# Kernel optimization log

Hardware: AMD Instinct MI355X
Metric: run time of the kernel (lower is better)

## Reference

```python
import jax, jax.numpy as jnp
import numpy as np

B = 4096
IND = 512
OUTD = 512
DEG = 2
P = 2  # dim_treat
KNOTS = [[0.33, 0.66], [0.33, 0.66]]
D = DEG + 1 + len(KNOTS[0])  # 5 basis functions per treatment dim


def setup_inputs() -> dict:
    key = jax.random.key(0)
    k1, k2, k3 = jax.random.split(key, 3)
    x = jax.random.uniform(k1, (B, P + IND), dtype=jnp.float32)  # treat dims in [0,1]
    weight = jax.random.uniform(k2, (IND, OUTD, D ** P), dtype=jnp.float32)  # torch.rand init
    bias = jax.random.uniform(k3, (OUTD, D ** P), dtype=jnp.float32)
    return {"x": x, "weight": weight, "bias": bias}


def _truncated_power_basis(x_treat):
    # x_treat: [B, P] -> basis: [B, P, D]
    knots = jnp.asarray(KNOTS, dtype=x_treat.dtype)  # [P, n_knots]
    # polynomial part: 1, x, x^2, ... x^DEG
    pows = jnp.stack([x_treat ** i for i in range(DEG + 1)], axis=-1)  # [B, P, DEG+1]
    # truncated part: relu(x - knot)^DEG  (DEG > 1 branch of original code)
    trunc = jax.nn.relu(x_treat[:, :, None] - knots[None, :, :]) ** DEG  # [B, P, n_knots]
    return jnp.concatenate([pows, trunc], axis=-1)


def reference(x, weight, bias):
    x_treat = x[:, :P]          # [B, P]
    x_feature = x[:, P:]        # [B, IND]
    basis = _truncated_power_basis(x_treat)  # [B, P, D]
    # Kronecker product across the two treatment dims: outer product, flattened
    kb = jnp.einsum('bi,bj->bij', basis[:, 0, :], basis[:, 1, :]).reshape(x.shape[0], D * P * 0 + D * D)  # [B, D^2]
    # fused: (weight^T @ x_feature) contracted with the per-sample basis coefficients
    out = jnp.einsum('bi,iod,bd->bo', x_feature, weight, kb)  # [B, OUTD]
    out = out + kb @ bias.T      # bias also varies with treatment basis
    out = jax.nn.relu(out)       # act='relu'
    # islastlayer=0: re-attach treatment dims
    return jnp.concatenate([x_treat, out], axis=1)  # [B, P + OUTD]
```

## Files before the change

kernel.cpp:

```cpp
#include <hip/hip_runtime.h>
#include <hip/hip_bf16.h>
#include <string.h>

#define NB    4096
#define IND_  512
#define OUTD_ 512
#define XCOLS 514
#define ND    25
#define KTOT  12800
#define KT2B  12928
#define NSPL  4

#define BM 128
#define BN 128
#define BKB 128

#define PWI 64
#define PWO 4
#define PWC (PWO * ND)
#define T8P 112

typedef float  f32x4  __attribute__((ext_vector_type(4)));
typedef int    i32x4  __attribute__((ext_vector_type(4)));
typedef int    i32x8  __attribute__((ext_vector_type(8)));
typedef unsigned short u16x4 __attribute__((ext_vector_type(4)));
typedef unsigned int   u32x2 __attribute__((ext_vector_type(2)));

__device__ __forceinline__ unsigned short f2bf(float f) {
  unsigned int x = __float_as_uint(f);
  return (unsigned short)((x + 0x7fffu + ((x >> 16) & 1u)) >> 16);
}

__device__ __forceinline__ float bf2f(unsigned short u) {
  return __uint_as_float(((unsigned int)u) << 16);
}

__device__ __forceinline__ unsigned int pk_bf16(float a, float b) {
  return (unsigned int)f2bf(a) | ((unsigned int)f2bf(b) << 16);
}

__device__ __forceinline__ unsigned char f2fp8(float v) {
  if (v < 0.015625f) {
    return (unsigned char)__float2int_rn(v * 512.0f);
  }
  unsigned int u = __float_as_uint(v);
  u += 0x7ffffu + ((u >> 20) & 1u);
  int e = (int)(u >> 23) - 127 + 7;
  unsigned int m = (u >> 20) & 7u;
  return (unsigned char)((e << 3) | m);
}

__device__ __forceinline__ float basis_f(float t, int j) {
  switch (j) {
    case 0: return 1.0f;
    case 1: return t;
    case 2: return t * t;
    case 3: { float r = t - 0.33f; r = r > 0.0f ? r : 0.0f; return r * r; }
    default:{ float r = t - 0.66f; r = r > 0.0f ? r : 0.0f; return r * r; }
  }
}

__device__ __forceinline__ void gload_lds16(const void* g, void* l) {
  __builtin_amdgcn_global_load_lds(
      (const __attribute__((address_space(1))) void*)g,
      (__attribute__((address_space(3))) void*)l, 16, 0, 0);
}

__device__ __forceinline__ void drain_all() {
  asm volatile("s_waitcnt vmcnt(0) lgkmcnt(0)" ::: "memory");
}

__global__ __launch_bounds__(256) void prep_all_kernel(
    const float* __restrict__ x, const float* __restrict__ W,
    const float* __restrict__ bias, unsigned char* __restrict__ Xf8,
    float* __restrict__ kb, unsigned char* __restrict__ kbT8,
    unsigned char* __restrict__ Wf8, float* __restrict__ out)
{
  __shared__ unsigned char tile8[PWI * T8P];
  const int bid = blockIdx.x;
  const int tid = threadIdx.x;

  if (bid < 512) {
    const int lane = tid & 63;
    #pragma unroll
    for (int rr = 0; rr < 2; ++rr) {
      const int b = bid * 8 + (tid >> 6) * 2 + rr;
      const float* xr = x + (size_t)b * XCOLS;
      const float* fp = xr + 2 + lane * 8;
      float2 a0 = *(const float2*)(fp + 0);
      float2 a1 = *(const float2*)(fp + 2);
      float2 a2 = *(const float2*)(fp + 4);
      float2 a3 = *(const float2*)(fp + 6);
      float xf[8] = {a0.x, a0.y, a1.x, a1.y, a2.x, a2.y, a3.x, a3.y};
      u32x2 pk;
      pk[0] = (unsigned int)f2fp8(xf[0]) | ((unsigned int)f2fp8(xf[1]) << 8) |
              ((unsigned int)f2fp8(xf[2]) << 16) | ((unsigned int)f2fp8(xf[3]) << 24);
      pk[1] = (unsigned int)f2fp8(xf[4]) | ((unsigned int)f2fp8(xf[5]) << 8) |
              ((unsigned int)f2fp8(xf[6]) << 16) | ((unsigned int)f2fp8(xf[7]) << 24);
      *reinterpret_cast<u32x2*>(Xf8 + (size_t)b * IND_ + lane * 8) = pk;

      float t0 = xr[0], t1 = xr[1];
      if (lane < 2) out[(size_t)b * XCOLS + lane] = (lane == 0) ? t0 : t1;
      {
        int d1 = lane / 5, d2 = lane - d1 * 5;
        float kv = basis_f(t0, d1) * basis_f(t1, d2);
        if (lane < ND) kb[(size_t)b * ND + lane] = kv;
      }
      {
        int ta = 2 * lane, tb = 2 * lane + 1;
        unsigned char ba = 0, bb = 0;
        if (ta < ND) { int d1 = ta / 5, d2 = ta - d1 * 5;
                       ba = f2fp8(basis_f(t0, d1) * basis_f(t1, d2)); }
        if (tb < ND) { int d1 = tb / 5, d2 = tb - d1 * 5;
                       bb = f2fp8(basis_f(t0, d1) * basis_f(t1, d2)); }
        *(unsigned short*)(kbT8 + (size_t)b * 128 + 2 * lane) =
            (unsigned short)ba | ((unsigned short)bb << 8);
      }
    }
  } else {
    const int pw = bid - 512;
    const int i0 = (pw & 7) * PWI;
    const int o0 = (pw >> 3) * PWO;

    for (int t = tid; t < PWI * (PWC / 4); t += 256) {
      int il = t / (PWC / 4);
      int c4 = t - il * (PWC / 4);
      float4 v = *(const float4*)(W + ((size_t)(i0 + il) * OUTD_ + o0) * ND + c4 * 4);
      unsigned int pk = (unsigned int)f2fp8(v.x) | ((unsigned int)f2fp8(v.y) << 8) |
                        ((unsigned int)f2fp8(v.z) << 16) | ((unsigned int)f2fp8(v.w) << 24);
      *(unsigned int*)&tile8[il * T8P + c4 * 4] = pk;
    }
    __syncthreads();

    for (int g = tid; g < PWC * (PWI / 8); g += 256) {
      int c  = g >> 3;
      int ig = g & 7;
      int d  = c % 25;
      int o_l = c / 25;
      unsigned long long v = 0;
      #pragma unroll
      for (int jj = 0; jj < 8; ++jj)
        v |= (unsigned long long)tile8[(ig * 8 + jj) * T8P + c] << (8 * jj);
      size_t rowb = (size_t)(o0 + o_l) * KT2B + (size_t)d * IND_ + i0;
      *reinterpret_cast<unsigned long long*>(Wf8 + rowb + ig * 8) = v;
    }

    if ((pw & 7) == 0) {
      int o = o0 + (tid >> 6);
      int p = tid & 63;
      int ta = 2 * p, tb = 2 * p + 1;
      unsigned char ba = (ta < ND) ? f2fp8(bias[o * ND + ta]) : (unsigned char)0;
      unsigned char bb = (tb < ND) ? f2fp8(bias[o * ND + tb]) : (unsigned char)0;
      *(unsigned short*)(Wf8 + (size_t)o * KT2B + KTOT + 2 * p) =
          (unsigned short)ba | ((unsigned short)bb << 8);
    }
  }
}

__global__ __launch_bounds__(256, 2) void gemm_mx_kernel(
    const unsigned char* __restrict__ Wf8, const unsigned char* __restrict__ Xf8,
    const float* __restrict__ kb, const unsigned char* __restrict__ kbT8,
    unsigned short* __restrict__ Pb)
{
  __shared__ unsigned char Als[2][BM * BKB];
  __shared__ unsigned char Bls[2][BN * BKB];

  const int tid  = threadIdx.x;
  const int lane = tid & 63;
  const int w    = tid >> 6;
  const int l15  = lane & 15;
  const int quad = lane >> 4;

  const int id  = blockIdx.x;
  const int xcd = id & 7;
  const int j   = id >> 3;
  const int bx  = j & 3;
  const int pg  = xcd * 16 + (j >> 2);
  const int by  = pg & 31;
  const int bz  = pg >> 5;

  const int o0 = bx * BM;
  const int b0 = by * BN;
  const int ks_begin = bz * 3200;
  const int ks_end   = (bz == 3) ? KT2B : ks_begin + 3200;
  const int nIter    = (ks_end - ks_begin) / BKB;

  const int o_off = (w & 1) * 64;
  const int b_off = (w >> 1) * 64;
  const int srow  = lane >> 3;
  const int scol  = ((lane & 7) ^ srow) * 16;
  const int r7    = l15 & 7;
  const int s0    = ((2 * quad) ^ r7) * 16;
  const int s1    = ((2 * quad + 1) ^ r7) * 16;

  f32x4 acc[4][4], fin[4][4];
  #pragma unroll
  for (int i = 0; i < 4; ++i)
    #pragma unroll
    for (int jj = 0; jj < 4; ++jj) { acc[i][jj] = (f32x4)0.0f; fin[i][jj] = (f32x4)0.0f; }

  float kv[4] = {1.0f, 1.0f, 1.0f, 1.0f};
  int cur_d = -1;

  auto issueAB = [&](int k0, int buf) {
    const int dd = k0 >> 9;
    #pragma unroll
    for (int c = 0; c < 4; ++c) {
      int chunk = w * 4 + c;
      int r = chunk * 8 + srow;
      gload_lds16(Wf8 + (size_t)(o0 + r) * KT2B + k0 + scol, &Als[buf][chunk * 1024]);
      const unsigned char* gb = (dd < ND)
          ? Xf8 + (size_t)(b0 + r) * IND_ + (k0 & 511) + scol
          : kbT8 + (size_t)(b0 + r) * 128 + scol;
      gload_lds16(gb, &Bls[buf][chunk * 1024]);
    }
  };

  issueAB(ks_begin, 0);
  drain_all();
  __syncthreads();

  for (int n = 0; n < nIter; ++n) {
    const int k0 = ks_begin + n * BKB;
    const int p  = n & 1;
    const int q  = p ^ 1;

    if (n + 1 < nIter) issueAB(k0 + BKB, q);

    const int d = k0 >> 9;
    if (d != cur_d) {
      if (cur_d >= 0) {
        #pragma unroll
        for (int nf = 0; nf < 4; ++nf)
          #pragma unroll
          for (int mf = 0; mf < 4; ++mf)
            #pragma unroll
            for (int r = 0; r < 4; ++r) {
              fin[mf][nf][r] += kv[nf] * acc[mf][nf][r];
              acc[mf][nf][r] = 0.0f;
            }
      }
      cur_d = d;
      if (d < ND) {
        #pragma unroll
        for (int nf = 0; nf < 4; ++nf)
          kv[nf] = kb[(size_t)(b0 + b_off + nf * 16 + l15) * ND + d];
      } else {
        #pragma unroll
        for (int nf = 0; nf < 4; ++nf) kv[nf] = 1.0f;
      }
    }

    {
      i32x8 af[4], bfr[4];
      #pragma unroll
      for (int mf = 0; mf < 4; ++mf) {
        int rb = (o_off + mf * 16 + l15) * BKB;
        i32x4 lo = *reinterpret_cast<const i32x4*>(&Als[p][rb + s0]);
        i32x4 hi = *reinterpret_cast<const i32x4*>(&Als[p][rb + s1]);
        i32x8 v;
        v[0] = lo[0]; v[1] = lo[1]; v[2] = lo[2]; v[3] = lo[3];
        v[4] = hi[0]; v[5] = hi[1]; v[6] = hi[2]; v[7] = hi[3];
        af[mf] = v;
      }
      #pragma unroll
      for (int nf = 0; nf < 4; ++nf) {
        int rb = (b_off + nf * 16 + l15) * BKB;
        i32x4 lo = *reinterpret_cast<const i32x4*>(&Bls[p][rb + s0]);
        i32x4 hi = *reinterpret_cast<const i32x4*>(&Bls[p][rb + s1]);
        i32x8 v;
        v[0] = lo[0]; v[1] = lo[1]; v[2] = lo[2]; v[3] = lo[3];
        v[4] = hi[0]; v[5] = hi[1]; v[6] = hi[2]; v[7] = hi[3];
        bfr[nf] = v;
      }
      #pragma unroll
      for (int mf = 0; mf < 4; ++mf)
        #pragma unroll
        for (int nf = 0; nf < 4; ++nf)
          acc[mf][nf] = __builtin_amdgcn_mfma_scale_f32_16x16x128_f8f6f4(
              af[mf], bfr[nf], acc[mf][nf],
              0, 0, 0, 0x7f7f7f7f, 0, 0x7f7f7f7f);
    }

    drain_all();
    __syncthreads();
  }

  #pragma unroll
  for (int nf = 0; nf < 4; ++nf)
    #pragma unroll
    for (int mf = 0; mf < 4; ++mf)
      #pragma unroll
      for (int r = 0; r < 4; ++r)
        fin[mf][nf][r] += kv[nf] * acc[mf][nf][r];

  unsigned short* Pz = Pb + (size_t)bz * NB * OUTD_;
  #pragma unroll
  for (int mf = 0; mf < 4; ++mf)
    #pragma unroll
    for (int nf = 0; nf < 4; ++nf) {
      int bg = b0 + b_off + nf * 16 + l15;
      int og = o0 + o_off + mf * 16 + quad * 4;
      u32x2 pk;
      pk[0] = pk_bf16(fin[mf][nf][0], fin[mf][nf][1]);
      pk[1] = pk_bf16(fin[mf][nf][2], fin[mf][nf][3]);
      *reinterpret_cast<u32x2*>(&Pz[(size_t)bg * OUTD_ + og]) = pk;
    }
}

__global__ __launch_bounds__(256) void epilogue_kernel(
    const unsigned short* __restrict__ Pb, float* __restrict__ out)
{
  const int idx = (blockIdx.x * 256 + threadIdx.x) * 4;
  const int b = idx >> 9;
  const int o = idx & 511;
  const size_t ps = (size_t)NB * OUTD_;
  float s[4] = {0.0f, 0.0f, 0.0f, 0.0f};
  #pragma unroll
  for (int z = 0; z < NSPL; ++z) {
    u16x4 v = *reinterpret_cast<const u16x4*>(&Pb[z * ps + idx]);
    #pragma unroll
    for (int e = 0; e < 4; ++e) s[e] += bf2f(v[e]);
  }
  float* op = out + (size_t)b * XCOLS + 2 + o;
  float2 lo, hi;
  lo.x = s[0] > 0.0f ? s[0] : 0.0f;
  lo.y = s[1] > 0.0f ? s[1] : 0.0f;
  hi.x = s[2] > 0.0f ? s[2] : 0.0f;
  hi.y = s[3] > 0.0f ? s[3] : 0.0f;
  *(float2*)op = lo;
  *(float2*)(op + 2) = hi;
}

extern "C" void kernel_launch(void* const* d_in, const int* in_sizes, int n_in,
                              void* d_out, int out_size, void* d_ws, size_t ws_size,
                              hipStream_t stream) {
  const float* x    = (const float*)d_in[0];
  const float* W    = (const float*)d_in[1];
  const float* bias = (const float*)d_in[2];
  float* out = (float*)d_out;
  char* ws = (char*)d_ws;

  const size_t xf_off  = 0;
  const size_t wf_off  = 2097152;
  const size_t kb_off  = wf_off + (size_t)OUTD_ * KT2B;
  const size_t kbt_off = kb_off + 409600;
  const size_t p_off   = kbt_off + (size_t)NB * 128;
  unsigned char* Xf8  = (unsigned char*)(ws + xf_off);
  unsigned char* Wf8  = (unsigned char*)(ws + wf_off);
  float* kb           = (float*)(ws + kb_off);
  unsigned char* kbT8 = (unsigned char*)(ws + kbt_off);
  unsigned short* Pb  = (unsigned short*)(ws + p_off);

  prep_all_kernel<<<1536, 256, 0, stream>>>(x, W, bias, Xf8, kb, kbT8, Wf8, out);
  gemm_mx_kernel<<<512, 256, 0, stream>>>(Wf8, Xf8, kb, kbT8, Pb);
  epilogue_kernel<<<(NB * OUTD_) / 1024, 256, 0, stream>>>(Pb, out);
}
```

Measured before the change: 127.3 us.

## Enlarge GEMM tile to 256x128 with 512 threads and peel bias tail

```diff
diff --git a/kernel.cpp b/kernel.cpp
--- a/kernel.cpp
+++ b/kernel.cpp
@@ -11,7 +11,7 @@
 #define KT2B  12928
 #define NSPL  4
 
-#define BM 128
+#define BM 256
 #define BN 128
 #define BKB 128
 
@@ -157,7 +157,7 @@
   }
 }
 
-__global__ __launch_bounds__(256, 2) void gemm_mx_kernel(
+__global__ __launch_bounds__(512, 2) void gemm_mx_kernel(
     const unsigned char* __restrict__ Wf8, const unsigned char* __restrict__ Xf8,
     const float* __restrict__ kb, const unsigned char* __restrict__ kbT8,
     unsigned short* __restrict__ Pb)
@@ -173,26 +173,36 @@
 
   const int id  = blockIdx.x;
   const int xcd = id & 7;
-  const int j   = id >> 3;
-  const int bx  = j & 3;
-  const int pg  = xcd * 16 + (j >> 2);
-  const int by  = pg & 31;
-  const int bz  = pg >> 5;
+  const int bx  = xcd & 1;
+  const int bz  = xcd >> 1;
+  const int by  = id >> 3;
 
   const int o0 = bx * BM;
   const int b0 = by * BN;
   const int ks_begin = bz * 3200;
-  const int ks_end   = (bz == 3) ? KT2B : ks_begin + 3200;
-  const int nIter    = (ks_end - ks_begin) / BKB;
-
-  const int o_off = (w & 1) * 64;
-  const int b_off = (w >> 1) * 64;
+  const bool tail = (bz == 3);
+
+  const int o_off = (w & 3) * 64;
+  const int b_off = (w >> 2) * 64;
   const int srow  = lane >> 3;
   const int scol  = ((lane & 7) ^ srow) * 16;
   const int r7    = l15 & 7;
   const int s0    = ((2 * quad) ^ r7) * 16;
   const int s1    = ((2 * quad + 1) ^ r7) * 16;
 
+  const unsigned char* aRow[4];
+  #pragma unroll
+  for (int c = 0; c < 4; ++c)
+    aRow[c] = Wf8 + (size_t)(o0 + (w * 4 + c) * 8 + srow) * KT2B + scol;
+  const unsigned char* bRow[2];
+  #pragma unroll
+  for (int c = 0; c < 2; ++c)
+    bRow[c] = Xf8 + (size_t)(b0 + (w * 2 + c) * 8 + srow) * IND_ + scol;
+  const unsigned char* tRow[2];
+  #pragma unroll
+  for (int c = 0; c < 2; ++c)
+    tRow[c] = kbT8 + (size_t)(b0 + (w * 2 + c) * 8 + srow) * 128 + scol;
+
   f32x4 acc[4][4], fin[4][4];
   #pragma unroll
   for (int i = 0; i < 4; ++i)
@@ -202,32 +212,39 @@
   float kv[4] = {1.0f, 1.0f, 1.0f, 1.0f};
   int cur_d = -1;
 
-  auto issueAB = [&](int k0, int buf) {
-    const int dd = k0 >> 9;
-    #pragma unroll
-    for (int c = 0; c < 4; ++c) {
-      int chunk = w * 4 + c;
-      int r = chunk * 8 + srow;
-      gload_lds16(Wf8 + (size_t)(o0 + r) * KT2B + k0 + scol, &Als[buf][chunk * 1024]);
-      const unsigned char* gb = (dd < ND)
-          ? Xf8 + (size_t)(b0 + r) * IND_ + (k0 & 511) + scol
-          : kbT8 + (size_t)(b0 + r) * 128 + scol;
-      gload_lds16(gb, &Bls[buf][chunk * 1024]);
-    }
+  auto issueAB = [&](int ao, int bcol, int buf) {
+    #pragma unroll
+    for (int c = 0; c < 4; ++c)
+      gload_lds16(aRow[c] + ao, &Als[buf][(w * 4 + c) * 1024]);
+    #pragma unroll
+    for (int c = 0; c < 2; ++c)
+      gload_lds16(bRow[c] + bcol, &Bls[buf][(w * 2 + c) * 1024]);
   };
 
-  issueAB(ks_begin, 0);
+  int ao   = ks_begin;
+  int bcol = ks_begin & 511;
+  issueAB(ao, bcol, 0);
   drain_all();
   __syncthreads();
 
-  for (int n = 0; n < nIter; ++n) {
-    const int k0 = ks_begin + n * BKB;
-    const int p  = n & 1;
-    const int q  = p ^ 1;
-
-    if (n + 1 < nIter) issueAB(k0 + BKB, q);
-
-    const int d = k0 >> 9;
+  for (int n = 0; n < 25; ++n) {
+    const int p = n & 1;
+    const int q = p ^ 1;
+
+    if (n < 24) {
+      ao += BKB;
+      bcol = (bcol + BKB) & 511;
+      issueAB(ao, bcol, q);
+    } else if (tail) {
+      #pragma unroll
+      for (int c = 0; c < 4; ++c)
+        gload_lds16(aRow[c] + KTOT, &Als[q][(w * 4 + c) * 1024]);
+      #pragma unroll
+      for (int c = 0; c < 2; ++c)
+        gload_lds16(tRow[c], &Bls[q][(w * 2 + c) * 1024]);
+    }
+
+    const int d = (ks_begin + n * BKB) >> 9;
     if (d != cur_d) {
       if (cur_d >= 0) {
         #pragma unroll
@@ -241,14 +258,9 @@
             }
       }
       cur_d = d;
-      if (d < ND) {
-        #pragma unroll
-        for (int nf = 0; nf < 4; ++nf)
-          kv[nf] = kb[(size_t)(b0 + b_off + nf * 16 + l15) * ND + d];
-      } else {
-        #pragma unroll
-        for (int nf = 0; nf < 4; ++nf) kv[nf] = 1.0f;
-      }
+      #pragma unroll
+      for (int nf = 0; nf < 4; ++nf)
+        kv[nf] = kb[(size_t)(b0 + b_off + nf * 16 + l15) * ND + d];
     }
 
     {
@@ -293,6 +305,37 @@
       #pragma unroll
       for (int r = 0; r < 4; ++r)
         fin[mf][nf][r] += kv[nf] * acc[mf][nf][r];
+
+  if (tail) {
+    i32x8 af[4], bfr[4];
+    #pragma unroll
+    for (int mf = 0; mf < 4; ++mf) {
+      int rb = (o_off + mf * 16 + l15) * BKB;
+      i32x4 lo = *reinterpret_cast<const i32x4*>(&Als[1][rb + s0]);
+      i32x4 hi = *reinterpret_cast<const i32x4*>(&Als[1][rb + s1]);
+      i32x8 v;
+      v[0] = lo[0]; v[1] = lo[1]; v[2] = lo[2]; v[3] = lo[3];
+      v[4] = hi[0]; v[5] = hi[1]; v[6] = hi[2]; v[7] = hi[3];
+      af[mf] = v;
+    }
+    #pragma unroll
+    for (int nf = 0; nf < 4; ++nf) {
+      int rb = (b_off + nf * 16 + l15) * BKB;
+      i32x4 lo = *reinterpret_cast<const i32x4*>(&Bls[1][rb + s0]);
+      i32x4 hi = *reinterpret_cast<const i32x4*>(&Bls[1][rb + s1]);
+      i32x8 v;
+      v[0] = lo[0]; v[1] = lo[1]; v[2] = lo[2]; v[3] = lo[3];
+      v[4] = hi[0]; v[5] = hi[1]; v[6] = hi[2]; v[7] = hi[3];
+      bfr[nf] = v;
+    }
+    #pragma unroll
+    for (int mf = 0; mf < 4; ++mf)
+      #pragma unroll
+      for (int nf = 0; nf < 4; ++nf)
+        fin[mf][nf] = __builtin_amdgcn_mfma_scale_f32_16x16x128_f8f6f4(
+            af[mf], bfr[nf], fin[mf][nf],
+            0, 0, 0, 0x7f7f7f7f, 0, 0x7f7f7f7f);
+  }
 
   unsigned short* Pz = Pb + (size_t)bz * NB * OUTD_;
   #pragma unroll
@@ -353,6 +396,6 @@
   unsigned short* Pb  = (unsigned short*)(ws + p_off);
 
   prep_all_kernel<<<1536, 256, 0, stream>>>(x, W, bias, Xf8, kb, kbT8, Wf8, out);
-  gemm_mx_kernel<<<512, 256, 0, stream>>>(Wf8, Xf8, kb, kbT8, Pb);
+  gemm_mx_kernel<<<256, 512, 0, stream>>>(Wf8, Xf8, kb, kbT8, Pb);
   epilogue_kernel<<<(NB * OUTD_) / 1024, 256, 0, stream>>>(Pb, out);
 }
```

New measurement: 130.3 us. 1.02x slower.

## Hold X tile in registers, split K by input chunk, use differenced basis weights

Applied to the files above, without the earlier changes.

```diff
diff --git a/kernel.cpp b/kernel.cpp
--- a/kernel.cpp
+++ b/kernel.cpp
@@ -11,9 +11,8 @@
 #define KT2B  12928
 #define NSPL  4
 
-#define BM 128
+#define BM 256
 #define BN 128
-#define BKB 128
 
 #define PWI 64
 #define PWO 4
@@ -60,20 +59,10 @@
   }
 }
 
-__device__ __forceinline__ void gload_lds16(const void* g, void* l) {
-  __builtin_amdgcn_global_load_lds(
-      (const __attribute__((address_space(1))) void*)g,
-      (__attribute__((address_space(3))) void*)l, 16, 0, 0);
-}
-
-__device__ __forceinline__ void drain_all() {
-  asm volatile("s_waitcnt vmcnt(0) lgkmcnt(0)" ::: "memory");
-}
-
 __global__ __launch_bounds__(256) void prep_all_kernel(
     const float* __restrict__ x, const float* __restrict__ W,
     const float* __restrict__ bias, unsigned char* __restrict__ Xf8,
-    float* __restrict__ kb, unsigned char* __restrict__ kbT8,
+    float* __restrict__ kbDT, unsigned char* __restrict__ kbT8,
     unsigned char* __restrict__ Wf8, float* __restrict__ out)
 {
   __shared__ unsigned char tile8[PWI * T8P];
@@ -103,8 +92,13 @@
       if (lane < 2) out[(size_t)b * XCOLS + lane] = (lane == 0) ? t0 : t1;
       {
         int d1 = lane / 5, d2 = lane - d1 * 5;
-        float kv = basis_f(t0, d1) * basis_f(t1, d2);
-        if (lane < ND) kb[(size_t)b * ND + lane] = kv;
+        float kvd = basis_f(t0, d1) * basis_f(t1, d2);
+        float kvn = 0.0f;
+        if (lane < 24) {
+          int e1 = (lane + 1) / 5, e2 = (lane + 1) - e1 * 5;
+          kvn = basis_f(t0, e1) * basis_f(t1, e2);
+        }
+        if (lane < ND) kbDT[(size_t)lane * NB + b] = kvd - kvn;
       }
       {
         int ta = 2 * lane, tb = 2 * lane + 1;
@@ -157,14 +151,11 @@
   }
 }
 
-__global__ __launch_bounds__(256, 2) void gemm_mx_kernel(
+__global__ __launch_bounds__(512, 2) void gemm_mx_kernel(
     const unsigned char* __restrict__ Wf8, const unsigned char* __restrict__ Xf8,
-    const float* __restrict__ kb, const unsigned char* __restrict__ kbT8,
+    const float* __restrict__ kbDT, const unsigned char* __restrict__ kbT8,
     unsigned short* __restrict__ Pb)
 {
-  __shared__ unsigned char Als[2][BM * BKB];
-  __shared__ unsigned char Bls[2][BN * BKB];
-
   const int tid  = threadIdx.x;
   const int lane = tid & 63;
   const int w    = tid >> 6;
@@ -172,135 +163,114 @@
   const int quad = lane >> 4;
 
   const int id  = blockIdx.x;
-  const int xcd = id & 7;
-  const int j   = id >> 3;
-  const int bx  = j & 3;
-  const int pg  = xcd * 16 + (j >> 2);
-  const int by  = pg & 31;
-  const int bz  = pg >> 5;
+  const int bx  = id & 1;
+  const int iw  = (id >> 1) & 3;
+  const int by  = id >> 3;
 
   const int o0 = bx * BM;
   const int b0 = by * BN;
-  const int ks_begin = bz * 3200;
-  const int ks_end   = (bz == 3) ? KT2B : ks_begin + 3200;
-  const int nIter    = (ks_end - ks_begin) / BKB;
-
-  const int o_off = (w & 1) * 64;
-  const int b_off = (w >> 1) * 64;
-  const int srow  = lane >> 3;
-  const int scol  = ((lane & 7) ^ srow) * 16;
-  const int r7    = l15 & 7;
-  const int s0    = ((2 * quad) ^ r7) * 16;
-  const int s1    = ((2 * quad + 1) ^ r7) * 16;
-
-  f32x4 acc[4][4], fin[4][4];
+  const bool tail = (iw == 3);
+
+  const int wr = w * 32;
+
+  auto load8 = [](const unsigned char* p) -> i32x8 {
+    i32x4 lo = *reinterpret_cast<const i32x4*>(p);
+    i32x4 hi = *reinterpret_cast<const i32x4*>(p + 16);
+    i32x8 v;
+    v[0] = lo[0]; v[1] = lo[1]; v[2] = lo[2]; v[3] = lo[3];
+    v[4] = hi[0]; v[5] = hi[1]; v[6] = hi[2]; v[7] = hi[3];
+    return v;
+  };
+
+  i32x8 bfr[8];
   #pragma unroll
-  for (int i = 0; i < 4; ++i)
-    #pragma unroll
-    for (int jj = 0; jj < 4; ++jj) { acc[i][jj] = (f32x4)0.0f; fin[i][jj] = (f32x4)0.0f; }
-
-  float kv[4] = {1.0f, 1.0f, 1.0f, 1.0f};
-  int cur_d = -1;
-
-  auto issueAB = [&](int k0, int buf) {
-    const int dd = k0 >> 9;
-    #pragma unroll
-    for (int c = 0; c < 4; ++c) {
-      int chunk = w * 4 + c;
-      int r = chunk * 8 + srow;
-      gload_lds16(Wf8 + (size_t)(o0 + r) * KT2B + k0 + scol, &Als[buf][chunk * 1024]);
-      const unsigned char* gb = (dd < ND)
-          ? Xf8 + (size_t)(b0 + r) * IND_ + (k0 & 511) + scol
-          : kbT8 + (size_t)(b0 + r) * 128 + scol;
-      gload_lds16(gb, &Bls[buf][chunk * 1024]);
-    }
+  for (int nf = 0; nf < 8; ++nf)
+    bfr[nf] = load8(Xf8 + (size_t)(b0 + nf * 16 + l15) * IND_ + iw * 128 + quad * 32);
+
+  const unsigned char* aP0 =
+      Wf8 + (size_t)(o0 + wr + l15) * KT2B + iw * 128 + quad * 32;
+  const unsigned char* aP1 = aP0 + (size_t)16 * KT2B;
+
+  const float* dkP = kbDT + b0 + l15;
+
+  f32x4 acc[2][8], fin[2][8];
+  #pragma unroll
+  for (int mf = 0; mf < 2; ++mf)
+    #pragma unroll
+    for (int nf = 0; nf < 8; ++nf) { acc[mf][nf] = (f32x4)0.0f; fin[mf][nf] = (f32x4)0.0f; }
+
+  auto mfma_flush = [&](const i32x8 (&a)[2], const float (&dk)[8]) {
+    #pragma unroll
+    for (int mf = 0; mf < 2; ++mf)
+      #pragma unroll
+      for (int nf = 0; nf < 8; ++nf)
+        acc[mf][nf] = __builtin_amdgcn_mfma_scale_f32_16x16x128_f8f6f4(
+            a[mf], bfr[nf], acc[mf][nf],
+            0, 0, 0, 0x7f7f7f7f, 0, 0x7f7f7f7f);
+    #pragma unroll
+    for (int mf = 0; mf < 2; ++mf)
+      #pragma unroll
+      for (int nf = 0; nf < 8; ++nf)
+        #pragma unroll
+        for (int r = 0; r < 4; ++r)
+          fin[mf][nf][r] += dk[nf] * acc[mf][nf][r];
   };
 
-  issueAB(ks_begin, 0);
-  drain_all();
-  __syncthreads();
-
-  for (int n = 0; n < nIter; ++n) {
-    const int k0 = ks_begin + n * BKB;
-    const int p  = n & 1;
-    const int q  = p ^ 1;
-
-    if (n + 1 < nIter) issueAB(k0 + BKB, q);
-
-    const int d = k0 >> 9;
-    if (d != cur_d) {
-      if (cur_d >= 0) {
-        #pragma unroll
-        for (int nf = 0; nf < 4; ++nf)
-          #pragma unroll
-          for (int mf = 0; mf < 4; ++mf)
-            #pragma unroll
-            for (int r = 0; r < 4; ++r) {
-              fin[mf][nf][r] += kv[nf] * acc[mf][nf][r];
-              acc[mf][nf][r] = 0.0f;
-            }
-      }
-      cur_d = d;
-      if (d < ND) {
-        #pragma unroll
-        for (int nf = 0; nf < 4; ++nf)
-          kv[nf] = kb[(size_t)(b0 + b_off + nf * 16 + l15) * ND + d];
-      } else {
-        #pragma unroll
-        for (int nf = 0; nf < 4; ++nf) kv[nf] = 1.0f;
-      }
-    }
-
-    {
-      i32x8 af[4], bfr[4];
+  i32x8 a0[2], a1[2];
+  a0[0] = load8(aP0);
+  a0[1] = load8(aP1);
+
+  for (int pass = 0; pass < 12; ++pass) {
+    a1[0] = load8(aP0 + 512);
+    a1[1] = load8(aP1 + 512);
+    float dka[8];
+    #pragma unroll
+    for (int nf = 0; nf < 8; ++nf) dka[nf] = dkP[nf * 16];
+    mfma_flush(a0, dka);
+
+    a0[0] = load8(aP0 + 1024);
+    a0[1] = load8(aP1 + 1024);
+    float dkb[8];
+    #pragma unroll
+    for (int nf = 0; nf < 8; ++nf) dkb[nf] = dkP[NB + nf * 16];
+    mfma_flush(a1, dkb);
+
+    aP0 += 1024; aP1 += 1024;
+    dkP += 2 * NB;
+  }
+
+  if (tail) {
+    a1[0] = load8(aP0 + 128);
+    a1[1] = load8(aP1 + 128);
+  }
+  {
+    float dkl[8];
+    #pragma unroll
+    for (int nf = 0; nf < 8; ++nf) dkl[nf] = dkP[nf * 16];
+    mfma_flush(a0, dkl);
+  }
+
+  if (tail) {
+    i32x8 bft[8];
+    #pragma unroll
+    for (int nf = 0; nf < 8; ++nf)
+      bft[nf] = load8(kbT8 + (size_t)(b0 + nf * 16 + l15) * 128 + quad * 32);
+    #pragma unroll
+    for (int mf = 0; mf < 2; ++mf)
       #pragma unroll
-      for (int mf = 0; mf < 4; ++mf) {
-        int rb = (o_off + mf * 16 + l15) * BKB;
-        i32x4 lo = *reinterpret_cast<const i32x4*>(&Als[p][rb + s0]);
-        i32x4 hi = *reinterpret_cast<const i32x4*>(&Als[p][rb + s1]);
-        i32x8 v;
-        v[0] = lo[0]; v[1] = lo[1]; v[2] = lo[2]; v[3] = lo[3];
-        v[4] = hi[0]; v[5] = hi[1]; v[6] = hi[2]; v[7] = hi[3];
-        af[mf] = v;
-      }
-      #pragma unroll
-      for (int nf = 0; nf < 4; ++nf) {
-        int rb = (b_off + nf * 16 + l15) * BKB;
-        i32x4 lo = *reinterpret_cast<const i32x4*>(&Bls[p][rb + s0]);
-        i32x4 hi = *reinterpret_cast<const i32x4*>(&Bls[p][rb + s1]);
-        i32x8 v;
-        v[0] = lo[0]; v[1] = lo[1]; v[2] = lo[2]; v[3] = lo[3];
-        v[4] = hi[0]; v[5] = hi[1]; v[6] = hi[2]; v[7] = hi[3];
-        bfr[nf] = v;
-      }
-      #pragma unroll
-      for (int mf = 0; mf < 4; ++mf)
-        #pragma unroll
-        for (int nf = 0; nf < 4; ++nf)
-          acc[mf][nf] = __builtin_amdgcn_mfma_scale_f32_16x16x128_f8f6f4(
-              af[mf], bfr[nf], acc[mf][nf],
-              0, 0, 0, 0x7f7f7f7f, 0, 0x7f7f7f7f);
-    }
-
-    drain_all();
-    __syncthreads();
-  }
-
+      for (int nf = 0; nf < 8; ++nf)
+        fin[mf][nf] = __builtin_amdgcn_mfma_scale_f32_16x16x128_f8f6f4(
+            a1[mf], bft[nf], fin[mf][nf],
+            0, 0, 0, 0x7f7f7f7f, 0, 0x7f7f7f7f);
+  }
+
+  unsigned short* Pz = Pb + (size_t)iw * NB * OUTD_;
   #pragma unroll
-  for (int nf = 0; nf < 4; ++nf)
-    #pragma unroll
-    for (int mf = 0; mf < 4; ++mf)
-      #pragma unroll
-      for (int r = 0; r < 4; ++r)
-        fin[mf][nf][r] += kv[nf] * acc[mf][nf][r];
-
-  unsigned short* Pz = Pb + (size_t)bz * NB * OUTD_;
-  #pragma unroll
-  for (int mf = 0; mf < 4; ++mf)
-    #pragma unroll
-    for (int nf = 0; nf < 4; ++nf) {
-      int bg = b0 + b_off + nf * 16 + l15;
-      int og = o0 + o_off + mf * 16 + quad * 4;
+  for (int mf = 0; mf < 2; ++mf)
+    #pragma unroll
+    for (int nf = 0; nf < 8; ++nf) {
+      int bg = b0 + nf * 16 + l15;
+      int og = o0 + wr + mf * 16 + quad * 4;
       u32x2 pk;
       pk[0] = pk_bf16(fin[mf][nf][0], fin[mf][nf][1]);
       pk[1] = pk_bf16(fin[mf][nf][2], fin[mf][nf][3]);
@@ -348,11 +318,11 @@
   const size_t p_off   = kbt_off + (size_t)NB * 128;
   unsigned char* Xf8  = (unsigned char*)(ws + xf_off);
   unsigned char* Wf8  = (unsigned char*)(ws + wf_off);
-  float* kb           = (float*)(ws + kb_off);
+  float* kbDT         = (float*)(ws + kb_off);
   unsigned char* kbT8 = (unsigned char*)(ws + kbt_off);
   unsigned short* Pb  = (unsigned short*)(ws + p_off);
 
-  prep_all_kernel<<<1536, 256, 0, stream>>>(x, W, bias, Xf8, kb, kbT8, Wf8, out);
-  gemm_mx_kernel<<<512, 256, 0, stream>>>(Wf8, Xf8, kb, kbT8, Pb);
+  prep_all_kernel<<<1536, 256, 0, stream>>>(x, W, bias, Xf8, kbDT, kbT8, Wf8, out);
+  gemm_mx_kernel<<<256, 512, 0, stream>>>(Wf8, Xf8, kbDT, kbT8, Pb);
   epilogue_kernel<<<(NB * OUTD_) / 1024, 256, 0, stream>>>(Pb, out);
 }
```

Measured after the change: 169.8 us. +33.4%, slower.
